# Optimization experiments

Measured on AMD Instinct MI355X. Metric: run time of the kernel, lower is better.

Reference implementation:

```python
import jax, jax.numpy as jnp
import numpy as np

SCALE = 4.0  # InputEmbedding scale


def setup_inputs() -> dict:
    key = jax.random.key(0)
    ks = jax.random.split(key, 16)
    T_obs, T_pred, N, E, H = 9, 12, 16384, 64, 128
    n_scenes = 512  # N / 32 tracks per scene
    inp = {
        "observed": jax.random.normal(ks[0], (T_obs, N, 2), jnp.float32),
        "prediction": jax.random.normal(ks[1], (T_pred, N, 2), jnp.float32),
        "goals": jax.random.normal(ks[2], (N, 2), jnp.float32),
        "batch_split": jnp.arange(0, N + 1, N // n_scenes, dtype=jnp.int64),
        # InputEmbedding: Linear(2 -> E)
        "W_emb": jax.random.normal(ks[3], (E, 2), jnp.float32) * 0.5,
        "b_emb": jax.random.normal(ks[4], (E,), jnp.float32) * 0.1,
        # LSTMCell(E -> H)
        "W_ih": jax.random.normal(ks[5], (4 * H, E), jnp.float32) * 0.08,
        "W_hh": jax.random.normal(ks[6], (4 * H, H), jnp.float32) * 0.08,
        "b_ih": jax.random.normal(ks[7], (4 * H,), jnp.float32) * 0.05,
        "b_hh": jax.random.normal(ks[8], (4 * H,), jnp.float32) * 0.05,
        # real_classifier MLP: [H, H/2, H/4, 1], ReLU after every Linear
        "W1": jax.random.normal(ks[9], (H // 2, H), jnp.float32) * 0.08,
        "b1": jnp.zeros((H // 2,), jnp.float32),
        "W2": jax.random.normal(ks[10], (H // 4, H // 2), jnp.float32) * 0.12,
        "b2": jnp.zeros((H // 4,), jnp.float32),
        "W3": jax.random.normal(ks[11], (1, H // 4), jnp.float32) * 0.2,
        "b3": jnp.zeros((1,), jnp.float32),
    }
    return inp


def _lstm_cell(x, h, c, W_ih, W_hh, b_ih, b_hh):
    gates = x @ W_ih.T + b_ih + h @ W_hh.T + b_hh  # [N, 4H]
    i, f, g, o = jnp.split(gates, 4, axis=-1)
    i = jax.nn.sigmoid(i)
    f = jax.nn.sigmoid(f)
    o = jax.nn.sigmoid(o)
    g = jnp.tanh(g)
    c2 = f * c + i * g
    h2 = o * jnp.tanh(c2)
    return h2, c2


def reference(observed, prediction, goals, batch_split,
              W_emb, b_emb, W_ih, W_hh, b_ih, b_hh,
              W1, b1, W2, b2, W3, b3):
    # pool=None, goal_flag=False -> step is: NaN-mask, velocity embed, LSTMCell,
    # masked write-back of (h, c) for valid tracks only.
    obs = jnp.concatenate([observed, prediction], axis=0)  # [T, N, 2]
    N = obs.shape[1]
    H = W_hh.shape[1]

    def step(carry, o12):
        h, c = carry
        o1, o2 = o12
        mask = ~(jnp.isnan(o1[:, 0]) | jnp.isnan(o2[:, 0]))  # [N]
        vel = jnp.where(mask[:, None], o2 - o1, 0.0)  # [N, 2]
        emb = (vel * SCALE) @ W_emb.T + b_emb  # [N, E]
        h2, c2 = _lstm_cell(emb, h, c, W_ih, W_hh, b_ih, b_hh)
        h = jnp.where(mask[:, None], h2, h)
        c = jnp.where(mask[:, None], c2, c)
        return (h, c), None

    h0 = jnp.zeros((N, H), obs.dtype)
    c0 = jnp.zeros((N, H), obs.dtype)
    (h, _c), _ = jax.lax.scan(step, (h0, c0), (obs[:-1], obs[1:]))

    primary = h[batch_split[:-1]]  # [batch_size, H]
    # make_mlp with relu appends ReLU after every Linear, including the last.
    x = jax.nn.relu(primary @ W1.T + b1)
    x = jax.nn.relu(x @ W2.T + b2)
    scores = jax.nn.relu(x @ W3.T + b3)  # [batch_size, 1]
    return scores
```

## Files before the change

### kernel.cpp

```cpp
#include <hip/hip_runtime.h>
#include <math.h>

#define SCALE 4.0f
#define H 128
#define E 64
#define NS 2
#define TMAX 32

#define WS_UC_OFF  131072

typedef _Float16 f16x8 __attribute__((ext_vector_type(8)));
typedef __attribute__((ext_vector_type(4))) float f32x4;

__device__ __forceinline__ bool is_nanf(float x) {
    return (__float_as_uint(x) & 0x7fffffffu) > 0x7f800000u;
}
__device__ __forceinline__ float rcpf(float x) { return __builtin_amdgcn_rcpf(x); }
__device__ __forceinline__ float sigm(float x) { return rcpf(1.0f + __expf(-x)); }
__device__ __forceinline__ float tanhfast(float x) {
    return fmaf(2.0f, rcpf(1.0f + __expf(-2.0f * x)), -1.0f);
}

__global__ __launch_bounds__(256)
void prep_kernel(const float* __restrict__ W_hh,
                 const float* __restrict__ W_ih,
                 const float* __restrict__ W_emb,
                 const float* __restrict__ b_emb,
                 const float* __restrict__ b_ih,
                 const float* __restrict__ b_hh,
                 char* __restrict__ ws)
{
    const int gid = blockIdx.x * 256 + threadIdx.x;
    if (gid < 8192) {
        const int lane = gid & 63;
        const int kb   = (gid >> 6) & 3;
        const int q    = (gid >> 8) & 3;
        const int w    = gid >> 10;
        const int mt   = q * 8 + w;
        const int row  = mt * 16 + (lane & 15);
        const int col0 = kb * 32 + (lane >> 4) * 8;
        const float* p = W_hh + (size_t)row * H + col0;
        f16x8 h8;
        #pragma unroll
        for (int j = 0; j < 8; ++j) h8[j] = (_Float16)p[j];
        *(f16x8*)(ws + (size_t)gid * 16) = h8;
    } else if (gid < 8192 + 512) {
        const int r = gid - 8192;
        const float* wr = W_ih + (size_t)r * E;
        float s0 = 0.f, s1 = 0.f, sc = 0.f;
        #pragma unroll 8
        for (int k = 0; k < E; ++k) {
            const float wv = wr[k];
            s0 += wv * W_emb[2 * k + 0];
            s1 += wv * W_emb[2 * k + 1];
            sc += wv * b_emb[k];
        }
        f32x4 v = {s0, s1, sc + b_ih[r] + b_hh[r], 0.0f};
        *(f32x4*)(ws + WS_UC_OFF + (size_t)r * 16) = v;
    }
}

__global__ __launch_bounds__(512, 2)
void lstm_disc_kernel(
    const float* __restrict__ observed,
    const float* __restrict__ prediction,
    const int* __restrict__ batch_split,
    const char* __restrict__ ws,
    const float* __restrict__ W1, const float* __restrict__ b1,
    const float* __restrict__ W2, const float* __restrict__ b2,
    const float* __restrict__ W3, const float* __restrict__ b3,
    float* __restrict__ out,
    int N, int T_obs, int T_total, int n_scenes)
{
    __shared__ __align__(16) _Float16 hb_hi[2][4][8][8];
    __shared__ __align__(16) _Float16 hb_lo[2][4][8][8];
    __shared__ float h32[NS][H];
    __shared__ float px[NS][TMAX], py[NS][TMAX];
    __shared__ float aA[NS][TMAX], bA[NS][TMAX];
    __shared__ int   mA[NS][TMAX];
    __shared__ float x1s[NS][H / 2];
    __shared__ float x2s[NS][H / 4];

    const int tid  = threadIdx.x;
    const int wave = tid >> 6;
    const int lane = tid & 63;
    const int ln15 = lane & 15;
    const int g4   = lane >> 4;
    const int es   = ln15 & 3;
    const int esc  = es & 1;
    const int ea   = ln15 >> 2;
    const int eu   = wave * 16 + g4 * 4 + ea;
    const int sc0  = blockIdx.x * NS;

    f16x8 ahi[4][4];
    #pragma unroll
    for (int q = 0; q < 4; ++q) {
        #pragma unroll
        for (int kb = 0; kb < 4; ++kb) {
            const size_t idx = ((size_t)((wave * 4 + q) * 4 + kb) * 64 + lane) * 16;
            ahi[q][kb] = *(const f16x8*)(ws + idx);
        }
    }
    float U0r[4], U1r[4], Ccr[4];
    #pragma unroll
    for (int q = 0; q < 4; ++q) {
        const f32x4 v = *(const f32x4*)(ws + WS_UC_OFF + (size_t)(eu + q * H) * 16);
        U0r[q] = v[0]; U1r[q] = v[1]; Ccr[q] = v[2];
    }

    if (tid < NS * TMAX) {
        const int s = tid >> 5, t = tid & 31;
        const int scene = sc0 + s;
        const int agent = (scene < n_scenes) ? batch_split[scene] : 0;
        if (t < T_total) {
            const float* src = (t < T_obs)
                ? (observed   + (size_t)t           * N * 2)
                : (prediction + (size_t)(t - T_obs) * N * 2);
            px[s][t] = src[(size_t)agent * 2 + 0];
            py[s][t] = src[(size_t)agent * 2 + 1];
        }
    }
    {
        int* zh = (int*)hb_hi;
        int* zl = (int*)hb_lo;
        if (tid < 256) { zh[tid] = 0; zl[tid] = 0; }
    }
    __syncthreads();

    if (tid < NS * TMAX) {
        const int s = tid >> 5, t = tid & 31;
        if (t < T_total - 1) {
            const bool m = !(is_nanf(px[s][t]) || is_nanf(px[s][t + 1]));
            aA[s][t] = m ? SCALE * (px[s][t + 1] - px[s][t]) : 0.0f;
            bA[s][t] = m ? SCALE * (py[s][t + 1] - py[s][t]) : 0.0f;
            mA[s][t] = m ? 1 : 0;
        }
    }

    const int wb_kb = eu >> 5;
    const int wb_ln = ((eu >> 3) & 3) + 4 * esc;
    const int wb_j  = eu & 7;
    const bool wb_on = (es < 2);

    float c_st = 0.0f, h_st = 0.0f;
    __syncthreads();

    for (int t = 0; t < T_total - 1; ++t) {
        const int rp = t & 1, wp = rp ^ 1;

        const float aa = aA[esc][t];
        const float bb = bA[esc][t];
        const int   mm = mA[esc][t];

        f16x8 bhi[4], blo[4];
        #pragma unroll
        for (int kb = 0; kb < 4; ++kb) {
            bhi[kb] = *(const f16x8*)&hb_hi[rp][kb][g4 + 4 * esc][0];
            blo[kb] = *(const f16x8*)&hb_lo[rp][kb][g4 + 4 * esc][0];
        }

        f32x4 accH[4], accL[4];
        #pragma unroll
        for (int q = 0; q < 4; ++q) {
            accH[q] = (f32x4){0.f, 0.f, 0.f, 0.f};
            accL[q] = (f32x4){0.f, 0.f, 0.f, 0.f};
        }
        #pragma unroll
        for (int kb = 0; kb < 4; ++kb) {
            #pragma unroll
            for (int q = 0; q < 4; ++q) {
                accH[q] = __builtin_amdgcn_mfma_f32_16x16x32_f16(ahi[q][kb], bhi[kb], accH[q], 0, 0, 0);
                accL[q] = __builtin_amdgcn_mfma_f32_16x16x32_f16(ahi[q][kb], blo[kb], accL[q], 0, 0, 0);
            }
        }

        const float p0 = accH[0][ea] + accL[0][ea] + Ccr[0] + aa * U0r[0] + bb * U1r[0];
        const float p1 = accH[1][ea] + accL[1][ea] + Ccr[1] + aa * U0r[1] + bb * U1r[1];
        const float p2 = accH[2][ea] + accL[2][ea] + Ccr[2] + aa * U0r[2] + bb * U1r[2];
        const float p3 = accH[3][ea] + accL[3][ea] + Ccr[3] + aa * U0r[3] + bb * U1r[3];
        const float ig = sigm(p0);
        const float fg = sigm(p1);
        const float gg = tanhfast(p2);
        const float og = sigm(p3);
        const float c2 = fg * c_st + ig * gg;
        const float h2 = og * tanhfast(c2);
        if (mm) { c_st = c2; h_st = h2; }

        if (wb_on) {
            const _Float16 hhi = (_Float16)h_st;
            const _Float16 hlo = (_Float16)(h_st - (float)hhi);
            hb_hi[wp][wb_kb][wb_ln][wb_j] = hhi;
            hb_lo[wp][wb_kb][wb_ln][wb_j] = hlo;
            if (t == T_total - 2) h32[esc][eu] = h_st;
        }
        __syncthreads();
    }

    if (tid < NS * (H / 2)) {
        const int s = tid >> 6, u = tid & 63;
        const float4* wr = (const float4*)(W1 + (size_t)u * H);
        const float4* hv = (const float4*)h32[s];
        float sum = b1[u];
        #pragma unroll
        for (int k = 0; k < H / 4; ++k) {
            const float4 w = wr[k], h = hv[k];
            sum += h.x * w.x + h.y * w.y + h.z * w.z + h.w * w.w;
        }
        x1s[s][u] = fmaxf(sum, 0.f);
    }
    __syncthreads();
    if (tid < NS * (H / 4)) {
        const int s = tid >> 5, u = tid & 31;
        const float4* wr = (const float4*)(W2 + (size_t)u * (H / 2));
        const float4* xv = (const float4*)x1s[s];
        float sum = b2[u];
        #pragma unroll
        for (int k = 0; k < H / 8; ++k) {
            const float4 w = wr[k], x = xv[k];
            sum += x.x * w.x + x.y * w.y + x.z * w.z + x.w * w.w;
        }
        x2s[s][u] = fmaxf(sum, 0.f);
    }
    __syncthreads();
    if (tid < NS) {
        const int scene = sc0 + tid;
        if (scene < n_scenes) {
            float sum = b3[0];
            #pragma unroll
            for (int k = 0; k < H / 4; ++k) sum += x2s[tid][k] * W3[k];
            out[scene] = fmaxf(sum, 0.f);
        }
    }
}

extern "C" void kernel_launch(void* const* d_in, const int* in_sizes, int n_in,
                              void* d_out, int out_size, void* d_ws, size_t ws_size,
                              hipStream_t stream) {
    const float* observed   = (const float*)d_in[0];
    const float* prediction = (const float*)d_in[1];
    const int*   batch_split = (const int*)d_in[3];
    const float* W_emb = (const float*)d_in[4];
    const float* b_emb = (const float*)d_in[5];
    const float* W_ih  = (const float*)d_in[6];
    const float* W_hh  = (const float*)d_in[7];
    const float* b_ih  = (const float*)d_in[8];
    const float* b_hh  = (const float*)d_in[9];
    const float* W1 = (const float*)d_in[10];
    const float* b1 = (const float*)d_in[11];
    const float* W2 = (const float*)d_in[12];
    const float* b2 = (const float*)d_in[13];
    const float* W3 = (const float*)d_in[14];
    const float* b3 = (const float*)d_in[15];
    float* out = (float*)d_out;

    const int N       = in_sizes[2] / 2;
    const int T_obs   = in_sizes[0] / (2 * N);
    const int T_total = T_obs + in_sizes[1] / (2 * N);
    const int n_scenes = in_sizes[3] - 1;

    prep_kernel<<<34, 256, 0, stream>>>(
        W_hh, W_ih, W_emb, b_emb, b_ih, b_hh, (char*)d_ws);

    const int nblocks = (n_scenes + NS - 1) / NS;
    lstm_disc_kernel<<<nblocks, 512, 0, stream>>>(
        observed, prediction, batch_split, (const char*)d_ws,
        W1, b1, W2, b2, W3, b3,
        out, N, T_obs, T_total, n_scenes);
}
```

Baseline: 111.8 us.

## Pack hi/lo fp16 split of h into MFMA columns, halve MFMA count

The hidden state is kept as an fp16 hi part plus an fp16 lo residual. Previously each was multiplied by W_hh in its own set of MFMAs (32 per step). The hi and lo parts now sit in separate columns of one B operand (hT layout), so 16 MFMAs per step cover both. The two partial sums are added with a ds_swizzle lane-xor. This cuts MFMA issue and LDS reads on the serial per-timestep critical path, at the cost of one cross-lane swizzle per gate and a different shared-memory layout.

```diff
diff --git a/kernel.cpp b/kernel.cpp
--- a/kernel.cpp
+++ b/kernel.cpp
@@ -19,6 +19,9 @@
 __device__ __forceinline__ float sigm(float x) { return rcpf(1.0f + __expf(-x)); }
 __device__ __forceinline__ float tanhfast(float x) {
     return fmaf(2.0f, rcpf(1.0f + __expf(-2.0f * x)), -1.0f);
+}
+__device__ __forceinline__ float swz_xor1(float v) {
+    return __int_as_float(__builtin_amdgcn_ds_swizzle(__float_as_int(v), 0x041F));
 }
 
 __global__ __launch_bounds__(256)
@@ -35,8 +38,8 @@
         const int lane = gid & 63;
         const int kb   = (gid >> 6) & 3;
         const int q    = (gid >> 8) & 3;
-        const int w    = gid >> 10;
-        const int mt   = q * 8 + w;
+        const int w8   = gid >> 10;
+        const int mt   = q * 8 + w8;
         const int row  = mt * 16 + (lane & 15);
         const int col0 = kb * 32 + (lane >> 4) * 8;
         const float* p = W_hh + (size_t)row * H + col0;
@@ -72,8 +75,7 @@
     float* __restrict__ out,
     int N, int T_obs, int T_total, int n_scenes)
 {
-    __shared__ __align__(16) _Float16 hb_hi[2][4][8][8];
-    __shared__ __align__(16) _Float16 hb_lo[2][4][8][8];
+    __shared__ __align__(16) _Float16 hT[2][4][4][32];
     __shared__ float h32[NS][H];
     __shared__ float px[NS][TMAX], py[NS][TMAX];
     __shared__ float aA[NS][TMAX], bA[NS][TMAX];
@@ -86,21 +88,22 @@
     const int lane = tid & 63;
     const int ln15 = lane & 15;
     const int g4   = lane >> 4;
-    const int es   = ln15 & 3;
-    const int esc  = es & 1;
-    const int ea   = ln15 >> 2;
-    const int eu   = wave * 16 + g4 * 4 + ea;
+    const int c    = ln15 & 3;
+    const int r    = ln15 >> 2;
+    const int esc  = c >> 1;
+    const int term = c & 1;
+    const int eu   = wave * 16 + g4 * 4 + r;
     const int sc0  = blockIdx.x * NS;
 
-    f16x8 ahi[4][4];
+    f16x8 afr[4][4];
     #pragma unroll
-    for (int q = 0; q < 4; ++q) {
+    for (int q = 0; q < 4; ++q)
         #pragma unroll
         for (int kb = 0; kb < 4; ++kb) {
-            const size_t idx = ((size_t)((wave * 4 + q) * 4 + kb) * 64 + lane) * 16;
-            ahi[q][kb] = *(const f16x8*)(ws + idx);
-        }
-    }
+            const size_t slot = ((size_t)((wave * 4 + q) * 4 + kb) * 64 + lane) * 16;
+            afr[q][kb] = *(const f16x8*)(ws + slot);
+        }
+
     float U0r[4], U1r[4], Ccr[4];
     #pragma unroll
     for (int q = 0; q < 4; ++q) {
@@ -120,11 +123,7 @@
             py[s][t] = src[(size_t)agent * 2 + 1];
         }
     }
-    {
-        int* zh = (int*)hb_hi;
-        int* zl = (int*)hb_lo;
-        if (tid < 256) { zh[tid] = 0; zl[tid] = 0; }
-    }
+    if (tid < 512) ((int*)hT)[tid] = 0;
     __syncthreads();
 
     if (tid < NS * TMAX) {
@@ -138,11 +137,9 @@
     }
 
     const int wb_kb = eu >> 5;
-    const int wb_ln = ((eu >> 3) & 3) + 4 * esc;
-    const int wb_j  = eu & 7;
-    const bool wb_on = (es < 2);
-
-    float c_st = 0.0f, h_st = 0.0f;
+    const int wb_k  = eu & 31;
+
+    float c_st = 0.f, h_st = 0.f;
     __syncthreads();
 
     for (int t = 0; t < T_total - 1; ++t) {
@@ -152,47 +149,39 @@
         const float bb = bA[esc][t];
         const int   mm = mA[esc][t];
 
-        f16x8 bhi[4], blo[4];
-        #pragma unroll
-        for (int kb = 0; kb < 4; ++kb) {
-            bhi[kb] = *(const f16x8*)&hb_hi[rp][kb][g4 + 4 * esc][0];
-            blo[kb] = *(const f16x8*)&hb_lo[rp][kb][g4 + 4 * esc][0];
-        }
-
-        f32x4 accH[4], accL[4];
+        f16x8 bf[4];
+        #pragma unroll
+        for (int kb = 0; kb < 4; ++kb)
+            bf[kb] = *(const f16x8*)&hT[rp][kb][c][g4 * 8];
+
+        f32x4 acc[4];
+        #pragma unroll
+        for (int q = 0; q < 4; ++q) acc[q] = (f32x4){0.f, 0.f, 0.f, 0.f};
+        #pragma unroll
+        for (int kb = 0; kb < 4; ++kb)
+            #pragma unroll
+            for (int q = 0; q < 4; ++q)
+                acc[q] = __builtin_amdgcn_mfma_f32_16x16x32_f16(afr[q][kb], bf[kb], acc[q], 0, 0, 0);
+
+        float p[4];
         #pragma unroll
         for (int q = 0; q < 4; ++q) {
-            accH[q] = (f32x4){0.f, 0.f, 0.f, 0.f};
-            accL[q] = (f32x4){0.f, 0.f, 0.f, 0.f};
-        }
-        #pragma unroll
-        for (int kb = 0; kb < 4; ++kb) {
-            #pragma unroll
-            for (int q = 0; q < 4; ++q) {
-                accH[q] = __builtin_amdgcn_mfma_f32_16x16x32_f16(ahi[q][kb], bhi[kb], accH[q], 0, 0, 0);
-                accL[q] = __builtin_amdgcn_mfma_f32_16x16x32_f16(ahi[q][kb], blo[kb], accL[q], 0, 0, 0);
-            }
-        }
-
-        const float p0 = accH[0][ea] + accL[0][ea] + Ccr[0] + aa * U0r[0] + bb * U1r[0];
-        const float p1 = accH[1][ea] + accL[1][ea] + Ccr[1] + aa * U0r[1] + bb * U1r[1];
-        const float p2 = accH[2][ea] + accL[2][ea] + Ccr[2] + aa * U0r[2] + bb * U1r[2];
-        const float p3 = accH[3][ea] + accL[3][ea] + Ccr[3] + aa * U0r[3] + bb * U1r[3];
-        const float ig = sigm(p0);
-        const float fg = sigm(p1);
-        const float gg = tanhfast(p2);
-        const float og = sigm(p3);
+            const float own = acc[q][r];
+            p[q] = own + swz_xor1(own) + Ccr[q] + aa * U0r[q] + bb * U1r[q];
+        }
+        const float ig = sigm(p[0]);
+        const float fg = sigm(p[1]);
+        const float gg = tanhfast(p[2]);
+        const float og = sigm(p[3]);
         const float c2 = fg * c_st + ig * gg;
         const float h2 = og * tanhfast(c2);
         if (mm) { c_st = c2; h_st = h2; }
 
-        if (wb_on) {
-            const _Float16 hhi = (_Float16)h_st;
-            const _Float16 hlo = (_Float16)(h_st - (float)hhi);
-            hb_hi[wp][wb_kb][wb_ln][wb_j] = hhi;
-            hb_lo[wp][wb_kb][wb_ln][wb_j] = hlo;
-            if (t == T_total - 2) h32[esc][eu] = h_st;
-        }
+        const _Float16 hhi = (_Float16)h_st;
+        const _Float16 wv  = term ? (_Float16)(h_st - (float)hhi) : hhi;
+        hT[wp][wb_kb][c][wb_k] = wv;
+        if (t == T_total - 2 && term == 0) h32[esc][eu] = h_st;
+
         __syncthreads();
     }
 
```

Result: faster. 103.2 us (-7.7%).
